# Optimization experiments

Hardware: AMD Instinct MI355X
Metric: run time of the kernel (lower is better)

## Reference

```python
import jax, jax.numpy as jnp
import numpy as np

SCALES = [2 ** i for i in range(11)]  # scales=10 -> [1,2,4,...,1024]


def _linear_upsample(x, N):
    """torch F.interpolate(mode='linear', align_corners=False) along last axis.
    x: (B, C, pn) -> (B, C, N)."""
    pn = x.shape[-1]
    scale = pn / N
    coords = (jnp.arange(N, dtype=x.dtype) + 0.5) * scale - 0.5
    coords = jnp.clip(coords, 0.0, pn - 1)
    i0 = jnp.floor(coords).astype(jnp.int32)
    i1 = jnp.minimum(i0 + 1, pn - 1)
    w = (coords - i0.astype(x.dtype))
    return x[..., i0] * (1.0 - w) + x[..., i1] * w


def setup_inputs() -> dict:
    key = jax.random.key(0)
    k1, k2 = jax.random.split(key)
    B, N, C, K = 32, 1024, 512, 4096
    f_BNC = jax.random.normal(k1, (B, N, C), dtype=jnp.float32)
    # torch init: uniform(-1/K, 1/K)
    codebook = (jax.random.uniform(k2, (K, C), dtype=jnp.float32) * 2.0 - 1.0) / K
    return {"f_BNC": f_BNC, "codebook": codebook}


def reference(f_BNC, codebook):
    f_BCN = jnp.transpose(f_BNC, (0, 2, 1))  # (B, C, N)
    B, C, N = f_BCN.shape
    f_ng = jax.lax.stop_gradient(f_BCN)      # f_no_grad
    f_rest = f_ng
    f_hat = jnp.zeros_like(f_ng)
    Wd = jax.lax.stop_gradient(codebook)     # embedding.weight.data for distances
    w_sq = jnp.sum(Wd * Wd, axis=1)          # (K,)
    SN = len(SCALES)
    commit = jnp.zeros((), dtype=f_BCN.dtype)
    qlat = jnp.zeros((), dtype=f_BCN.dtype)
    for pn in SCALES:
        # area downsample: exact block mean since N % pn == 0
        r = f_rest.reshape(B, C, pn, N // pn).mean(axis=-1)        # (B, C, pn)
        z = jnp.transpose(r, (0, 2, 1)).reshape(B * pn, C)          # (B*pn, C)
        d = jnp.sum(z * z, axis=1, keepdims=True) + w_sq - 2.0 * (z @ Wd.T)  # (B*pn, K)
        p = jax.nn.softmax(d, axis=-1)
        h = (p @ codebook).reshape(B, pn, C)                        # soft codebook lookup
        h = jnp.transpose(h, (0, 2, 1))                             # (B, C, pn)
        h = _linear_upsample(h, N)                                  # (B, C, N)
        f_hat = f_hat + h
        f_rest = f_rest - h
        commit = commit + 0.25 * jnp.mean((jax.lax.stop_gradient(f_hat) - f_BCN) ** 2)
        qlat = qlat + jnp.mean((f_hat - f_ng) ** 2)
    commit = commit / SN
    qlat = qlat / SN
    # straight-through estimator
    f_hat_st = jax.lax.stop_gradient(f_hat) - f_ng + f_BCN
    return jnp.transpose(f_hat_st, (0, 2, 1)), commit, qlat
```

## Files before the change

### kernel.cpp

```cpp
#include <hip/hip_runtime.h>
#include <hip/hip_bf16.h>

constexpr int B = 32, N = 1024, C = 512, K = 4096, SN = 11;
constexpr long BCN = (long)B * N * C;
constexpr int TKC = 128;
constexpr int NCH = K / TKC;
constexpr float PSCALE = 256.f;
constexpr int SCONE = 0x7f7f7f7f;

typedef __attribute__((ext_vector_type(4))) float f32x4;
typedef __attribute__((ext_vector_type(16))) float f32x16;
typedef __attribute__((ext_vector_type(8))) int i32x8;
typedef __attribute__((ext_vector_type(4))) int i32x4;
typedef unsigned int u32;
typedef unsigned long u64;

union v32u {
  i32x8 v;
  i32x4 h[2];
};

static __device__ __forceinline__ short f2bf(float x) {
  __hip_bfloat16 h = __float2bfloat16(x);
  short s;
  __builtin_memcpy(&s, &h, sizeof(s));
  return s;
}
static __device__ __forceinline__ float bf2f(short s) {
  u32 u = ((u32)(unsigned short)s) << 16;
  float f;
  __builtin_memcpy(&f, &u, 4);
  return f;
}
static __device__ __forceinline__ u32 pk4_fp8(float a, float b, float c, float d) {
  int r = __builtin_amdgcn_cvt_pk_fp8_f32(a, b, 0, false);
  r = __builtin_amdgcn_cvt_pk_fp8_f32(c, d, r, true);
  return (u32)r;
}
static __device__ __forceinline__ f32x16 zero16() {
  f32x16 z;
#pragma unroll
  for (int i = 0; i < 16; ++i) z[i] = 0.f;
  return z;
}

__global__ __launch_bounds__(256) void wsq_kernel(const float* __restrict__ W,
                                                  float* __restrict__ wsq) {
  __shared__ float red[256];
  int k = blockIdx.x;
  const float* row = W + (long)k * C;
  float s = 0.f;
  for (int c = threadIdx.x; c < C; c += 256) {
    float v = row[c];
    s += v * v;
  }
  red[threadIdx.x] = s;
  __syncthreads();
  for (int off = 128; off > 0; off >>= 1) {
    if (threadIdx.x < off) red[threadIdx.x] += red[threadIdx.x + off];
    __syncthreads();
  }
  if (threadIdx.x == 0) wsq[k] = red[0];
}

__global__ __launch_bounds__(256) void colsum_kernel(const float* __restrict__ W,
                                                     float* __restrict__ csum) {
  int ch = blockIdx.x;
  const float* base = W + (long)ch * TKC * C;
  float s0 = 0.f, s1 = 0.f;
  for (int k = 0; k < TKC; ++k) {
    s0 += base[(long)k * C + threadIdx.x];
    s1 += base[(long)k * C + threadIdx.x + 256];
  }
  csum[ch * C + threadIdx.x] = s0;
  csum[ch * C + threadIdx.x + 256] = s1;
}

__global__ __launch_bounds__(256) void prep_w(const float* __restrict__ W,
                                              unsigned char* __restrict__ WnA,
                                              unsigned char* __restrict__ WtB) {
  __shared__ __attribute__((aligned(16))) unsigned char tile[32 * 520];
  const int blk = blockIdx.x, tid = threadIdx.x;
  const float* src = W + (long)blk * 32 * C;
#pragma unroll
  for (int i = 0; i < 16; ++i) {
    int idx = tid + i * 256;
    float4 v = ((const float4*)src)[idx];
    int key = idx >> 7, c = (idx & 127) * 4;
    *(u32*)&tile[key * 520 + c] = pk4_fp8(v.x, v.y, v.z, v.w);
  }
  __syncthreads();
#pragma unroll
  for (int i = 0; i < 2; ++i) {
    int slot = tid + i * 256;
    int cc = slot >> 6, L = slot & 63;
    const unsigned char* sp = &tile[(L & 31) * 520 + cc * 64 + (L >> 5) * 32];
    u64* dst = (u64*)(WnA + ((long)(blk * 8 + cc) * 64 + L) * 32);
    dst[0] = *(const u64*)(sp);
    dst[1] = *(const u64*)(sp + 8);
    dst[2] = *(const u64*)(sp + 16);
    dst[3] = *(const u64*)(sp + 24);
  }
#pragma unroll
  for (int i = 0; i < 2; ++i) {
    int slot = tid + i * 256;
    int c2 = slot >> 5, rho = slot & 31;
    union { unsigned char v[32]; u64 q[4]; } t;
#pragma unroll
    for (int j = 0; j < 32; ++j) t.v[j] = tile[j * 520 + c2 * 32 + rho];
    u64* dst = (u64*)(WtB + ((long)((blk >> 1) * 16 + c2) * 64 + (blk & 1) * 32 + rho) * 32);
    dst[0] = t.q[0]; dst[1] = t.q[1]; dst[2] = t.q[2]; dst[3] = t.q[3];
  }
}

__global__ __launch_bounds__(256) void init_f(const float* __restrict__ f,
                                              short* __restrict__ fbf,
                                              float* __restrict__ zpart) {
  int b = blockIdx.x >> 5;
  int n0 = (blockIdx.x & 31) * 32 + (threadIdx.x >> 7) * 16;
  int c4 = threadIdx.x & 127;
  float ax = 0, ay = 0, az = 0, aw = 0;
  for (int j = 0; j < 16; ++j) {
    long e = ((long)b * N + n0 + j) * 128 + c4;
    float4 v = ((const float4*)f)[e];
    short4 o = {f2bf(v.x), f2bf(v.y), f2bf(v.z), f2bf(v.w)};
    ((short4*)fbf)[e] = o;
    ax += v.x; ay += v.y; az += v.z; aw += v.w;
  }
  float4 zp = {ax, ay, az, aw};
  ((float4*)zpart)[((long)b * 64 + (n0 >> 4)) * 128 + c4] = zp;
}

__global__ __launch_bounds__(256) void reduce_zpart(const float* __restrict__ zpart,
                                                    unsigned char* __restrict__ zq, int pn) {
  long idx = (long)blockIdx.x * 256 + threadIdx.x;
  long tot = (long)B * pn * 128;
  if (idx >= tot) return;
  int c4 = (int)(idx & 127);
  long row = idx >> 7;
  int b = (int)(row / pn), j = (int)(row % pn);
  int r = 64 / pn;
  float ax = 0, ay = 0, az = 0, aw = 0;
  for (int i = 0; i < r; ++i) {
    float4 v = ((const float4*)zpart)[((long)b * 64 + j * r + i) * 128 + c4];
    ax += v.x; ay += v.y; az += v.z; aw += v.w;
  }
  float inv = (float)pn / (float)N;
  *(u32*)&zq[row * C + c4 * 4] = pk4_fp8(ax * inv, ay * inv, az * inv, aw * inv);
}

__global__ __launch_bounds__(256, 2) void flash_mfma(
    const unsigned char* __restrict__ zq, const unsigned char* __restrict__ WnA,
    const unsigned char* __restrict__ WtB, const float* __restrict__ wsq,
    const float* __restrict__ csum, short* __restrict__ hb,
    float* __restrict__ lpart, int M, int KS) {
  __shared__ __attribute__((aligned(16))) unsigned char ZS[16 * 2048];
  __shared__ __attribute__((aligned(16))) unsigned char PS[2][4 * 2048];
  const int tid = threadIdx.x;
  const int w = tid >> 6, lane = tid & 63;
  const int rho = lane & 31, hi = lane >> 5;
  const long row0 = (long)blockIdx.x * 64;
  const int nc = NCH / KS, ch0 = blockIdx.y * nc;
  const int lswz = (lane * 32) ^ (((lane >> 2) & 7) << 4);

#pragma unroll
  for (int i = 0; i < 4; ++i) {
    int u = i * 4 + w, zt = u >> 3, cc = u & 7;
    long row = row0 + zt * 32 + rho;
    i32x4 v0 = {0, 0, 0, 0}, v1 = {0, 0, 0, 0};
    if (row < M) {
      const i32x4* sp = (const i32x4*)(zq + row * C + cc * 64 + hi * 32);
      v0 = sp[0];
      v1 = sp[1];
    }
    *(i32x4*)(ZS + u * 2048 + lswz) = v0;
    *(i32x4*)(ZS + u * 2048 + (lswz ^ 16)) = v1;
  }
  f32x16 hacc[2][4];
#pragma unroll
  for (int zt = 0; zt < 2; ++zt)
#pragma unroll
    for (int ct = 0; ct < 4; ++ct) hacc[zt][ct] = zero16();
  float lreg[2] = {0.f, 0.f};
  float cs[4] = {0.f, 0.f, 0.f, 0.f};
  __syncthreads();

#pragma unroll 1
  for (int ci = 0; ci < nc; ++ci) {
    const int ch = ch0 + ci;
#pragma unroll
    for (int ct = 0; ct < 4; ++ct) cs[ct] += csum[ch * C + w * 128 + ct * 32 + rho];
    f32x16 s[2];
    s[0] = zero16();
    s[1] = zero16();
    const unsigned char* wa = WnA + ((long)(ch * 4 + w) * 8) * 2048 + lane * 32;
    const unsigned char* zb0 = ZS + lswz;
    const unsigned char* zb1 = ZS + (lswz ^ 16);
#pragma unroll
    for (int cc = 0; cc < 8; ++cc) {
      i32x8 a = *(const i32x8*)(wa + cc * 2048);
      v32u b0, b1;
      b0.h[0] = *(const i32x4*)(zb0 + cc * 2048);
      b0.h[1] = *(const i32x4*)(zb1 + cc * 2048);
      b1.h[0] = *(const i32x4*)(zb0 + (8 + cc) * 2048);
      b1.h[1] = *(const i32x4*)(zb1 + (8 + cc) * 2048);
      s[0] = __builtin_amdgcn_mfma_scale_f32_32x32x64_f8f6f4(a, b0.v, s[0], 0, 0, 0, SCONE, 0, SCONE);
      s[1] = __builtin_amdgcn_mfma_scale_f32_32x32x64_f8f6f4(a, b1.v, s[1], 0, 0, 0, SCONE, 0, SCONE);
    }
    const float* wsb = wsq + ch * TKC + w * 32 + hi * 4;
    float wv[16];
#pragma unroll
    for (int g = 0; g < 4; ++g) {
      float4 t = *(const float4*)(wsb + 8 * g);
      wv[4 * g + 0] = t.x; wv[4 * g + 1] = t.y; wv[4 * g + 2] = t.z; wv[4 * g + 3] = t.w;
    }
    unsigned char* Pun = PS[ci & 1] + (w >> 1) * 2048;
    const int pbase = (w & 1) * 1024 + rho * 32 + hi * 4;
    const int xP = ((rho >> 2) & 7) << 4;
#pragma unroll
    for (int zt = 0; zt < 2; ++zt) {
      float sum = 0.f, pv[16];
#pragma unroll
      for (int r = 0; r < 16; ++r) {
        float e = __expf(wv[r] - 2.f * s[zt][r]);
        sum += e;
        pv[r] = PSCALE * e - PSCALE;
      }
      lreg[zt] += sum;
#pragma unroll
      for (int g = 0; g < 4; ++g) {
        u32 pk = pk4_fp8(pv[4 * g], pv[4 * g + 1], pv[4 * g + 2], pv[4 * g + 3]);
        *(u32*)(Pun + zt * 4096 + ((pbase + 8 * g) ^ xP)) = pk;
      }
    }
    __syncthreads();
    const unsigned char* Pr0 = PS[ci & 1] + lswz;
    const unsigned char* Pr1 = PS[ci & 1] + (lswz ^ 16);
    i32x8 pa[2][2];
#pragma unroll
    for (int zt = 0; zt < 2; ++zt)
#pragma unroll
      for (int f = 0; f < 2; ++f) {
        v32u p;
        p.h[0] = *(const i32x4*)(Pr0 + (zt * 2 + f) * 2048);
        p.h[1] = *(const i32x4*)(Pr1 + (zt * 2 + f) * 2048);
        pa[zt][f] = p.v;
      }
    const unsigned char* wb = WtB + ((long)(ch * 2) * 16 + w * 4) * 2048 + lane * 32;
#pragma unroll
    for (int f = 0; f < 2; ++f)
#pragma unroll
      for (int ct = 0; ct < 4; ++ct) {
        i32x8 bw = *(const i32x8*)(wb + (f * 16 + ct) * 2048);
        hacc[0][ct] = __builtin_amdgcn_mfma_scale_f32_32x32x64_f8f6f4(pa[0][f], bw, hacc[0][ct], 0, 0, 0, SCONE, 0, SCONE);
        hacc[1][ct] = __builtin_amdgcn_mfma_scale_f32_32x32x64_f8f6f4(pa[1][f], bw, hacc[1][ct], 0, 0, 0, SCONE, 0, SCONE);
      }
  }
  __syncthreads();
  lreg[0] += __shfl_xor(lreg[0], 32);
  lreg[1] += __shfl_xor(lreg[1], 32);
  float* l4 = (float*)PS;
  if (hi == 0) {
    l4[rho * 4 + w] = lreg[0];
    l4[(32 + rho) * 4 + w] = lreg[1];
  }
  __syncthreads();
  constexpr float PINV = 1.f / PSCALE;
  if (KS == 1) {
#pragma unroll
    for (int zt = 0; zt < 2; ++zt)
#pragma unroll
      for (int r = 0; r < 16; ++r) {
        int rr = zt * 32 + (r & 3) + 8 * (r >> 2) + 4 * hi;
        long row = row0 + rr;
        if (row < M) {
          float4 lv = ((const float4*)l4)[rr];
          float inv = 1.f / (lv.x + lv.y + lv.z + lv.w);
#pragma unroll
          for (int ct = 0; ct < 4; ++ct)
            hb[row * C + w * 128 + ct * 32 + rho] =
                f2bf((cs[ct] + hacc[zt][ct][r] * PINV) * inv);
        }
      }
  } else {
    long base = (long)blockIdx.y * M * C;
#pragma unroll
    for (int zt = 0; zt < 2; ++zt)
#pragma unroll
      for (int r = 0; r < 16; ++r) {
        int rr = zt * 32 + (r & 3) + 8 * (r >> 2) + 4 * hi;
        long row = row0 + rr;
        if (row < M) {
#pragma unroll
          for (int ct = 0; ct < 4; ++ct)
            hb[base + row * C + w * 128 + ct * 32 + rho] =
                f2bf(cs[ct] + hacc[zt][ct][r] * PINV);
        }
      }
    if (w == 0) {
      long row = row0 + lane;
      if (row < M) {
        float4 lv = ((const float4*)l4)[lane];
        lpart[(long)blockIdx.y * M + row] = lv.x + lv.y + lv.z + lv.w;
      }
    }
  }
}

__global__ __launch_bounds__(256) void combine_kernel(short* __restrict__ hb,
                                                      const float* __restrict__ lpart,
                                                      int M, int KS) {
  long idx = (long)blockIdx.x * 256 + threadIdx.x;
  long tot = (long)M * 128;
  if (idx >= tot) return;
  int m = (int)(idx >> 7);
  float lsum = 0.f;
  for (int s = 0; s < KS; ++s) lsum += lpart[(long)s * M + m];
  float ax = 0, ay = 0, az = 0, aw = 0;
  for (int s = 0; s < KS; ++s) {
    short4 v = ((const short4*)hb)[(long)s * tot + idx];
    ax += bf2f(v.x); ay += bf2f(v.y); az += bf2f(v.z); aw += bf2f(v.w);
  }
  float inv = 1.f / lsum;
  short4 o = {f2bf(ax * inv), f2bf(ay * inv), f2bf(az * inv), f2bf(aw * inv)};
  ((short4*)hb)[idx] = o;
}

__global__ __launch_bounds__(256) void fused_up(
    const short* __restrict__ hb, const short* __restrict__ fbf,
    const short* fhin, short* fhout, float* __restrict__ outf,
    unsigned char* __restrict__ zq, float* __restrict__ zpart,
    double* __restrict__ accum, int pn, int pn_next, int first, int last) {
  const int b = blockIdx.x >> 5;
  const int n0 = (blockIdx.x & 31) * 32 + (threadIdx.x >> 7) * 16;
  const int c4 = threadIdx.x & 127;
  const float scale = (float)pn * (1.f / (float)N);
  const int bs_next = pn_next ? (N / pn_next) : 0;
  float zx = 0, zy = 0, zz = 0, zw = 0, part = 0.f;
  for (int j = 0; j < 16; ++j) {
    int n = n0 + j;
    long e = ((long)b * N + n) * 128 + c4;
    float coords = ((float)n + 0.5f) * scale - 0.5f;
    coords = fminf(fmaxf(coords, 0.f), (float)(pn - 1));
    int i0 = (int)coords;
    int i1 = min(i0 + 1, pn - 1);
    float wq = coords - (float)i0, ow = 1.f - wq;
    short4 h0 = ((const short4*)hb)[((long)b * pn + i0) * 128 + c4];
    short4 h1 = ((const short4*)hb)[((long)b * pn + i1) * 128 + c4];
    short4 fv = ((const short4*)fbf)[e];
    float fhx, fhy, fhz, fhw;
    if (first) {
      fhx = fhy = fhz = fhw = 0.f;
    } else {
      short4 p = ((const short4*)fhin)[e];
      fhx = bf2f(p.x); fhy = bf2f(p.y); fhz = bf2f(p.z); fhw = bf2f(p.w);
    }
    fhx += bf2f(h0.x) * ow + bf2f(h1.x) * wq;
    fhy += bf2f(h0.y) * ow + bf2f(h1.y) * wq;
    fhz += bf2f(h0.z) * ow + bf2f(h1.z) * wq;
    fhw += bf2f(h0.w) * ow + bf2f(h1.w) * wq;
    if (last) {
      float4 o = {fhx, fhy, fhz, fhw};
      ((float4*)outf)[e] = o;
    } else {
      short4 o = {f2bf(fhx), f2bf(fhy), f2bf(fhz), f2bf(fhw)};
      ((short4*)fhout)[e] = o;
    }
    float dx = fhx - bf2f(fv.x), dy = fhy - bf2f(fv.y);
    float dz = fhz - bf2f(fv.z), dw = fhw - bf2f(fv.w);
    part += dx * dx + dy * dy + dz * dz + dw * dw;
    zx -= dx; zy -= dy; zz -= dz; zw -= dw;
    if (pn_next >= 64) {
      if (((n + 1) & (bs_next - 1)) == 0) {
        float inv = 1.f / (float)bs_next;
        *(u32*)&zq[((long)b * pn_next + n / bs_next) * C + c4 * 4] =
            pk4_fp8(zx * inv, zy * inv, zz * inv, zw * inv);
        zx = zy = zz = zw = 0.f;
      }
    }
  }
  if (pn_next && pn_next < 64) {
    float4 zp = {zx, zy, zz, zw};
    ((float4*)zpart)[((long)b * 64 + (n0 >> 4)) * 128 + c4] = zp;
  }
  __shared__ float red[256];
  red[threadIdx.x] = part;
  __syncthreads();
  for (int off = 128; off > 0; off >>= 1) {
    if (threadIdx.x < off) red[threadIdx.x] += red[threadIdx.x + off];
    __syncthreads();
  }
  if (threadIdx.x == 0) atomicAdd(&accum[blockIdx.x & 255], (double)red[0]);
}

__global__ void finalize_kernel(const double* __restrict__ accum,
                                float* __restrict__ out_scalars) {
  if (threadIdx.x == 0 && blockIdx.x == 0) {
    double s = 0.0;
    for (int i = 0; i < 256; ++i) s += accum[i];
    double denom = (double)SN * (double)BCN;
    out_scalars[0] = (float)(0.25 * s / denom);
    out_scalars[1] = (float)(s / denom);
  }
}

extern "C" void kernel_launch(void* const* d_in, const int* in_sizes, int n_in,
                              void* d_out, int out_size, void* d_ws, size_t ws_size,
                              hipStream_t stream) {
  const float* f = (const float*)d_in[0];
  const float* W = (const float*)d_in[1];
  float* out = (float*)d_out;

  const long MBy = 1l << 20;
  char* ws = (char*)d_ws;
  short* hb = (short*)ws;
  short* fbf = (short*)(ws + 32 * MBy);
  short* fhbf = (short*)(ws + 64 * MBy);
  unsigned char* zq = (unsigned char*)(ws + 96 * MBy);
  unsigned char* WnA = (unsigned char*)(ws + 112 * MBy);
  unsigned char* WtB = (unsigned char*)(ws + 114 * MBy);
  float* zpart = (float*)(ws + 116 * MBy);
  float* wsqf = (float*)(ws + 120 * MBy);
  float* csum = (float*)(ws + 120 * MBy + (1l << 16));
  float* lpart = (float*)(ws + 120 * MBy + (1l << 17));
  double* accum = (double*)(ws + 121 * MBy);

  hipMemsetAsync(accum, 0, 256 * sizeof(double), stream);

  wsq_kernel<<<K, 256, 0, stream>>>(W, wsqf);
  colsum_kernel<<<NCH, 256, 0, stream>>>(W, csum);
  prep_w<<<K / 32, 256, 0, stream>>>(W, WnA, WtB);
  init_f<<<B * 32, 256, 0, stream>>>(f, fbf, zpart);
  reduce_zpart<<<(B * 128 + 255) / 256, 256, 0, stream>>>(zpart, zq, 1);

  for (int s = 0; s < SN; ++s) {
    int pn = 1 << s;
    int M = B * pn;
    int gx = (M + 63) / 64;
    int KS = 512 / gx;
    if (KS < 1) KS = 1;
    if (KS > 32) KS = 32;
    flash_mfma<<<dim3(gx, KS), 256, 0, stream>>>(zq, WnA, WtB, wsqf, csum, hb, lpart, M, KS);
    if (KS > 1)
      combine_kernel<<<(int)(((long)M * 128 + 255) / 256), 256, 0, stream>>>(hb, lpart, M, KS);
    int pn_next = (s < SN - 1) ? (pn << 1) : 0;
    fused_up<<<B * 32, 256, 0, stream>>>(hb, fbf, fhbf, fhbf, out, zq, zpart, accum,
                                         pn, pn_next, s == 0 ? 1 : 0, s == SN - 1 ? 1 : 0);
    if (pn_next && pn_next < 64)
      reduce_zpart<<<(int)(((long)B * pn_next * 128 + 255) / 256), 256, 0, stream>>>(zpart, zq, pn_next);
  }

  finalize_kernel<<<1, 64, 0, stream>>>(accum, out + BCN);
}
```

Before: 936.8 us.

## Shrink flash_mfma row tile to 32 rows and raise occupancy to 4 blocks

Halves the per-block row tile from 64 to 32 rows, which halves the shared memory and accumulator registers per block and allows 4 blocks per CU through the launch bounds. The grid is adjusted to M/32 blocks with a target of 1024 total blocks for the split-K factor, and the row bounds checks are dropped because M is always a multiple of 32. The aim is more parallelism and occupancy in the small-scale stages. In exchange, each block reuses codebook tiles across half as many rows, so traffic to the codebook in global memory or L2 roughly doubles.

After: 1.063 ms. 1.13x slower.

```diff
diff --git a/kernel.cpp b/kernel.cpp
--- a/kernel.cpp
+++ b/kernel.cpp
@@ -149,39 +149,32 @@
   *(u32*)&zq[row * C + c4 * 4] = pk4_fp8(ax * inv, ay * inv, az * inv, aw * inv);
 }
 
-__global__ __launch_bounds__(256, 2) void flash_mfma(
+__global__ __launch_bounds__(256, 4) void flash_mfma(
     const unsigned char* __restrict__ zq, const unsigned char* __restrict__ WnA,
     const unsigned char* __restrict__ WtB, const float* __restrict__ wsq,
     const float* __restrict__ csum, short* __restrict__ hb,
     float* __restrict__ lpart, int M, int KS) {
-  __shared__ __attribute__((aligned(16))) unsigned char ZS[16 * 2048];
-  __shared__ __attribute__((aligned(16))) unsigned char PS[2][4 * 2048];
+  __shared__ __attribute__((aligned(16))) unsigned char ZS[8 * 2048];
+  __shared__ __attribute__((aligned(16))) unsigned char PS[2][2 * 2048];
   const int tid = threadIdx.x;
   const int w = tid >> 6, lane = tid & 63;
   const int rho = lane & 31, hi = lane >> 5;
-  const long row0 = (long)blockIdx.x * 64;
+  const long row0 = (long)blockIdx.x * 32;
   const int nc = NCH / KS, ch0 = blockIdx.y * nc;
   const int lswz = (lane * 32) ^ (((lane >> 2) & 7) << 4);
 
 #pragma unroll
-  for (int i = 0; i < 4; ++i) {
-    int u = i * 4 + w, zt = u >> 3, cc = u & 7;
-    long row = row0 + zt * 32 + rho;
-    i32x4 v0 = {0, 0, 0, 0}, v1 = {0, 0, 0, 0};
-    if (row < M) {
-      const i32x4* sp = (const i32x4*)(zq + row * C + cc * 64 + hi * 32);
-      v0 = sp[0];
-      v1 = sp[1];
-    }
+  for (int i = 0; i < 2; ++i) {
+    int u = w * 2 + i;
+    const i32x4* sp = (const i32x4*)(zq + (row0 + rho) * C + u * 64 + hi * 32);
+    i32x4 v0 = sp[0], v1 = sp[1];
     *(i32x4*)(ZS + u * 2048 + lswz) = v0;
     *(i32x4*)(ZS + u * 2048 + (lswz ^ 16)) = v1;
   }
-  f32x16 hacc[2][4];
-#pragma unroll
-  for (int zt = 0; zt < 2; ++zt)
-#pragma unroll
-    for (int ct = 0; ct < 4; ++ct) hacc[zt][ct] = zero16();
-  float lreg[2] = {0.f, 0.f};
+  f32x16 hacc[4];
+#pragma unroll
+  for (int ct = 0; ct < 4; ++ct) hacc[ct] = zero16();
+  float lreg = 0.f;
   float cs[4] = {0.f, 0.f, 0.f, 0.f};
   __syncthreads();
 
@@ -190,22 +183,17 @@
     const int ch = ch0 + ci;
 #pragma unroll
     for (int ct = 0; ct < 4; ++ct) cs[ct] += csum[ch * C + w * 128 + ct * 32 + rho];
-    f32x16 s[2];
-    s[0] = zero16();
-    s[1] = zero16();
+    f32x16 s = zero16();
     const unsigned char* wa = WnA + ((long)(ch * 4 + w) * 8) * 2048 + lane * 32;
     const unsigned char* zb0 = ZS + lswz;
     const unsigned char* zb1 = ZS + (lswz ^ 16);
 #pragma unroll
     for (int cc = 0; cc < 8; ++cc) {
       i32x8 a = *(const i32x8*)(wa + cc * 2048);
-      v32u b0, b1;
-      b0.h[0] = *(const i32x4*)(zb0 + cc * 2048);
-      b0.h[1] = *(const i32x4*)(zb1 + cc * 2048);
-      b1.h[0] = *(const i32x4*)(zb0 + (8 + cc) * 2048);
-      b1.h[1] = *(const i32x4*)(zb1 + (8 + cc) * 2048);
-      s[0] = __builtin_amdgcn_mfma_scale_f32_32x32x64_f8f6f4(a, b0.v, s[0], 0, 0, 0, SCONE, 0, SCONE);
-      s[1] = __builtin_amdgcn_mfma_scale_f32_32x32x64_f8f6f4(a, b1.v, s[1], 0, 0, 0, SCONE, 0, SCONE);
+      v32u b;
+      b.h[0] = *(const i32x4*)(zb0 + cc * 2048);
+      b.h[1] = *(const i32x4*)(zb1 + cc * 2048);
+      s = __builtin_amdgcn_mfma_scale_f32_32x32x64_f8f6f4(a, b.v, s, 0, 0, 0, SCONE, 0, SCONE);
     }
     const float* wsb = wsq + ch * TKC + w * 32 + hi * 4;
     float wv[16];
@@ -214,95 +202,74 @@
       float4 t = *(const float4*)(wsb + 8 * g);
       wv[4 * g + 0] = t.x; wv[4 * g + 1] = t.y; wv[4 * g + 2] = t.z; wv[4 * g + 3] = t.w;
     }
+    float sum = 0.f, pv[16];
+#pragma unroll
+    for (int r = 0; r < 16; ++r) {
+      float e = __expf(wv[r] - 2.f * s[r]);
+      sum += e;
+      pv[r] = PSCALE * e - PSCALE;
+    }
+    lreg += sum;
     unsigned char* Pun = PS[ci & 1] + (w >> 1) * 2048;
     const int pbase = (w & 1) * 1024 + rho * 32 + hi * 4;
     const int xP = ((rho >> 2) & 7) << 4;
 #pragma unroll
-    for (int zt = 0; zt < 2; ++zt) {
-      float sum = 0.f, pv[16];
-#pragma unroll
-      for (int r = 0; r < 16; ++r) {
-        float e = __expf(wv[r] - 2.f * s[zt][r]);
-        sum += e;
-        pv[r] = PSCALE * e - PSCALE;
-      }
-      lreg[zt] += sum;
-#pragma unroll
-      for (int g = 0; g < 4; ++g) {
-        u32 pk = pk4_fp8(pv[4 * g], pv[4 * g + 1], pv[4 * g + 2], pv[4 * g + 3]);
-        *(u32*)(Pun + zt * 4096 + ((pbase + 8 * g) ^ xP)) = pk;
-      }
+    for (int g = 0; g < 4; ++g) {
+      u32 pk = pk4_fp8(pv[4 * g], pv[4 * g + 1], pv[4 * g + 2], pv[4 * g + 3]);
+      *(u32*)(Pun + ((pbase + 8 * g) ^ xP)) = pk;
     }
     __syncthreads();
     const unsigned char* Pr0 = PS[ci & 1] + lswz;
     const unsigned char* Pr1 = PS[ci & 1] + (lswz ^ 16);
-    i32x8 pa[2][2];
-#pragma unroll
-    for (int zt = 0; zt < 2; ++zt)
-#pragma unroll
-      for (int f = 0; f < 2; ++f) {
-        v32u p;
-        p.h[0] = *(const i32x4*)(Pr0 + (zt * 2 + f) * 2048);
-        p.h[1] = *(const i32x4*)(Pr1 + (zt * 2 + f) * 2048);
-        pa[zt][f] = p.v;
-      }
+    i32x8 pa[2];
+#pragma unroll
+    for (int f = 0; f < 2; ++f) {
+      v32u p;
+      p.h[0] = *(const i32x4*)(Pr0 + f * 2048);
+      p.h[1] = *(const i32x4*)(Pr1 + f * 2048);
+      pa[f] = p.v;
+    }
     const unsigned char* wb = WtB + ((long)(ch * 2) * 16 + w * 4) * 2048 + lane * 32;
 #pragma unroll
     for (int f = 0; f < 2; ++f)
 #pragma unroll
       for (int ct = 0; ct < 4; ++ct) {
         i32x8 bw = *(const i32x8*)(wb + (f * 16 + ct) * 2048);
-        hacc[0][ct] = __builtin_amdgcn_mfma_scale_f32_32x32x64_f8f6f4(pa[0][f], bw, hacc[0][ct], 0, 0, 0, SCONE, 0, SCONE);
-        hacc[1][ct] = __builtin_amdgcn_mfma_scale_f32_32x32x64_f8f6f4(pa[1][f], bw, hacc[1][ct], 0, 0, 0, SCONE, 0, SCONE);
+        hacc[ct] = __builtin_amdgcn_mfma_scale_f32_32x32x64_f8f6f4(pa[f], bw, hacc[ct], 0, 0, 0, SCONE, 0, SCONE);
       }
   }
   __syncthreads();
-  lreg[0] += __shfl_xor(lreg[0], 32);
-  lreg[1] += __shfl_xor(lreg[1], 32);
+  lreg += __shfl_xor(lreg, 32);
   float* l4 = (float*)PS;
-  if (hi == 0) {
-    l4[rho * 4 + w] = lreg[0];
-    l4[(32 + rho) * 4 + w] = lreg[1];
-  }
+  if (hi == 0) l4[rho * 4 + w] = lreg;
   __syncthreads();
   constexpr float PINV = 1.f / PSCALE;
   if (KS == 1) {
 #pragma unroll
-    for (int zt = 0; zt < 2; ++zt)
-#pragma unroll
-      for (int r = 0; r < 16; ++r) {
-        int rr = zt * 32 + (r & 3) + 8 * (r >> 2) + 4 * hi;
-        long row = row0 + rr;
-        if (row < M) {
-          float4 lv = ((const float4*)l4)[rr];
-          float inv = 1.f / (lv.x + lv.y + lv.z + lv.w);
-#pragma unroll
-          for (int ct = 0; ct < 4; ++ct)
-            hb[row * C + w * 128 + ct * 32 + rho] =
-                f2bf((cs[ct] + hacc[zt][ct][r] * PINV) * inv);
-        }
-      }
+    for (int r = 0; r < 16; ++r) {
+      int rr = (r & 3) + 8 * (r >> 2) + 4 * hi;
+      long row = row0 + rr;
+      float4 lv = ((const float4*)l4)[rr];
+      float inv = 1.f / (lv.x + lv.y + lv.z + lv.w);
+#pragma unroll
+      for (int ct = 0; ct < 4; ++ct)
+        hb[row * C + w * 128 + ct * 32 + rho] =
+            f2bf((cs[ct] + hacc[ct][r] * PINV) * inv);
+    }
   } else {
     long base = (long)blockIdx.y * M * C;
 #pragma unroll
-    for (int zt = 0; zt < 2; ++zt)
-#pragma unroll
-      for (int r = 0; r < 16; ++r) {
-        int rr = zt * 32 + (r & 3) + 8 * (r >> 2) + 4 * hi;
-        long row = row0 + rr;
-        if (row < M) {
-#pragma unroll
-          for (int ct = 0; ct < 4; ++ct)
-            hb[base + row * C + w * 128 + ct * 32 + rho] =
-                f2bf(cs[ct] + hacc[zt][ct][r] * PINV);
-        }
-      }
-    if (w == 0) {
-      long row = row0 + lane;
-      if (row < M) {
-        float4 lv = ((const float4*)l4)[lane];
-        lpart[(long)blockIdx.y * M + row] = lv.x + lv.y + lv.z + lv.w;
-      }
+    for (int r = 0; r < 16; ++r) {
+      int rr = (r & 3) + 8 * (r >> 2) + 4 * hi;
+      long row = row0 + rr;
+#pragma unroll
+      for (int ct = 0; ct < 4; ++ct)
+        hb[base + row * C + w * 128 + ct * 32 + rho] =
+            f2bf(cs[ct] + hacc[ct][r] * PINV);
+    }
+    if (w == 0 && lane < 32) {
+      float4 lv = ((const float4*)l4)[lane];
+      lpart[(long)blockIdx.y * M + row0 + lane] = lv.x + lv.y + lv.z + lv.w;
     }
   }
 }
@@ -436,8 +403,8 @@
   for (int s = 0; s < SN; ++s) {
     int pn = 1 << s;
     int M = B * pn;
-    int gx = (M + 63) / 64;
-    int KS = 512 / gx;
+    int gx = M / 32;
+    int KS = 1024 / gx;
     if (KS < 1) KS = 1;
     if (KS > 32) KS = 32;
     flash_mfma<<<dim3(gx, KS), 256, 0, stream>>>(zq, WnA, WtB, wsqf, csum, hb, lpart, M, KS);
```
